# Kernel tuning notes

Hardware: AMD Instinct MI355X
Metric: run time of the kernel (lower is better)

## Reference

```python
import jax, jax.numpy as jnp
import numpy as np

ALPHA = 0.2
NEG = -9e15


def gat_layer(h, adj, W, a):
    # h: [B,N,Fin], adj: [B,N,N], W: [Fin,Fout], a: [2*Fout,1]
    Wh = jnp.matmul(h, W)                       # [B,N,Fout]
    Fout = W.shape[1]
    a1 = a[:Fout, 0]                             # source part
    a2 = a[Fout:, 0]                             # target part
    # e_ij = LeakyReLU(a1.Wh_i + a2.Wh_j) -- avoids O(N^2*2F) concat
    e = jax.nn.leaky_relu(
        (Wh @ a1)[:, :, None] + (Wh @ a2)[:, None, :], negative_slope=ALPHA
    )                                            # [B,N,N]
    att = jax.nn.softmax(jnp.where(adj > 0, e, NEG), axis=2)
    return jnp.matmul(att, Wh)                  # [B,N,Fout]


def setup_inputs() -> dict:
    key = jax.random.key(0)
    ks = jax.random.split(key, 6)
    B, N, F_IN, F_HID, F_OUT, H = 16, 1024, 256, 64, 64, 4
    x = jax.random.normal(ks[0], (B, N, F_IN), dtype=jnp.float32)
    adj = jax.random.randint(ks[1], (B, N, N), 0, 2, dtype=jnp.int32)
    W_heads = jax.random.normal(ks[2], (H, F_IN, F_HID), dtype=jnp.float32) * 0.1
    a_heads = jax.random.normal(ks[3], (H, 2 * F_HID, 1), dtype=jnp.float32) * 0.1
    W_out = jax.random.normal(ks[4], (H * F_HID, F_OUT), dtype=jnp.float32) * 0.1
    a_out = jax.random.normal(ks[5], (2 * F_OUT, 1), dtype=jnp.float32) * 0.1
    return {"x": x, "adj": adj, "W_heads": W_heads, "a_heads": a_heads,
            "W_out": W_out, "a_out": a_out}


def reference(x, adj, W_heads, a_heads, W_out, a_out):
    # multi-head: vmap over heads -> [H,B,N,F_hid]
    heads = jax.vmap(lambda W, a: gat_layer(x, adj, W, a))(W_heads, a_heads)
    H, B, N, Fh = heads.shape
    h_cat = jnp.transpose(heads, (1, 2, 0, 3)).reshape(B, N, H * Fh)
    out = jax.nn.elu(gat_layer(h_cat, adj, W_out, a_out))  # [B,N,nclass]
    return jnp.mean(out, axis=1)                           # [B,nclass]
```

## Files before the change

### kernel.cpp

```cpp
#include <hip/hip_runtime.h>
#include <math.h>

#define BB 16
#define NN 1024
#define FH 64
#define NH 4
#define LOG2E 1.4426950408889634f

typedef __attribute__((ext_vector_type(8))) short short8;
typedef __attribute__((ext_vector_type(4))) float f32x4;
typedef __attribute__((ext_vector_type(4))) unsigned u32x4;
typedef unsigned long long u64;
typedef unsigned short ushort_t;

__device__ inline unsigned f2bf(float x) {
    unsigned u = __builtin_bit_cast(unsigned, x);
    u += 0x7fff + ((u >> 16) & 1);
    return u >> 16;
}
__device__ inline unsigned pkbf(float lo, float hi) {
    unsigned r;
    asm("v_cvt_pk_bf16_f32 %0, %1, %2" : "=v"(r) : "v"(lo), "v"(hi));
    return r;
}
__device__ inline float bf2f(short v) {
    return __builtin_bit_cast(float, (unsigned)((unsigned short)v) << 16);
}

__global__ void pack_kernel(const int* __restrict__ adj, u64* __restrict__ bm,
                            const float* __restrict__ Whd, const float* __restrict__ Wo,
                            ushort_t* __restrict__ BT1, ushort_t* __restrict__ BT2,
                            float* __restrict__ outz) {
    const int row = blockIdx.x * 4 + (threadIdx.x >> 6);
    const int lane = threadIdx.x & 63;
    const int* __restrict__ ar = adj + (size_t)row * NN;
    #pragma unroll
    for (int g = 0; g < 16; ++g) {
        u64 m = __ballot(ar[g * 64 + lane] > 0);
        if (lane == 0) bm[row * 16 + g] = m;
    }
    const int col = blockIdx.x, k = threadIdx.x;
    if (col < 256)      BT1[col * 256 + k] = (ushort_t)f2bf(Whd[(col >> 6) * 16384 + k * 64 + (col & 63)]);
    else if (col < 320) BT2[(col - 256) * 256 + k] = (ushort_t)f2bf(Wo[k * 64 + (col - 256)]);
    if (col == 0) {
        #pragma unroll
        for (int i = 0; i < 4; ++i) outz[i * 256 + k] = 0.f;
    }
}

template <int A_BF16>
__global__ __launch_bounds__(256, 4) void gemm_fused(
    const void* __restrict__ Ap, const ushort_t* __restrict__ BT,
    const float* __restrict__ av, ushort_t* __restrict__ WhbT,
    float* __restrict__ s1, float* __restrict__ s2, const int S) {
    constexpr int K = 256;
    __shared__ __align__(16) short tbuf[64][72];
    const int tid = threadIdx.x;
    const int w = tid >> 6, l = tid & 63, lo = l & 15, kg = l >> 4;

    const int nx = gridDim.x;
    const int id = blockIdx.y * nx + blockIdx.x;
    const int nwg = nx * gridDim.y;
    const int lid = (id & 7) * (nwg >> 3) + (id >> 3);
    const int row0 = (lid / nx) * 64, col0 = (lid % nx) * 64;

    const int b = row0 >> 10, j0 = row0 & (NN - 1);
    const int hsel = col0 >> 6;

    f32x4 acc[4];
    #pragma unroll
    for (int cb = 0; cb < 4; ++cb) acc[cb] = (f32x4){0.f, 0.f, 0.f, 0.f};

    if (A_BF16) {
        const ushort_t* __restrict__ arow = (const ushort_t*)Ap + (size_t)(row0 + w * 16 + lo) * K;
        #pragma unroll
        for (int ks = 0; ks < 8; ++ks) {
            const int k0 = ks * 32 + kg * 8;
            const short8 af = *(const short8*)(arow + k0);
            #pragma unroll
            for (int cb = 0; cb < 4; ++cb) {
                const short8 bf = *(const short8*)(BT + (size_t)(col0 + cb * 16 + lo) * K + k0);
                acc[cb] = __builtin_amdgcn_mfma_f32_16x16x32_bf16(af, bf, acc[cb], 0, 0, 0);
            }
        }
    } else {
        const float* __restrict__ arow = (const float*)Ap + (size_t)(row0 + w * 16 + lo) * K;
        #pragma unroll
        for (int ks = 0; ks < 8; ++ks) {
            const int k0 = ks * 32 + kg * 8;
            const float4 a0 = *(const float4*)(arow + k0);
            const float4 a1 = *(const float4*)(arow + k0 + 4);
            u32x4 ap;
            ap[0] = pkbf(a0.x, a0.y); ap[1] = pkbf(a0.z, a0.w);
            ap[2] = pkbf(a1.x, a1.y); ap[3] = pkbf(a1.z, a1.w);
            const short8 af = __builtin_bit_cast(short8, ap);
            #pragma unroll
            for (int cb = 0; cb < 4; ++cb) {
                const short8 bf = *(const short8*)(BT + (size_t)(col0 + cb * 16 + lo) * K + k0);
                acc[cb] = __builtin_amdgcn_mfma_f32_16x16x32_bf16(af, bf, acc[cb], 0, 0, 0);
            }
        }
    }

    float a1v[4], a2v[4];
    #pragma unroll
    for (int cb = 0; cb < 4; ++cb) {
        a1v[cb] = av[hsel * 128 + cb * 16 + lo];
        a2v[cb] = av[hsel * 128 + 64 + cb * 16 + lo];
    }
    float sp1[4], sp2[4];
    #pragma unroll
    for (int r = 0; r < 4; ++r) {
        sp1[r] = acc[0][r] * a1v[0] + acc[1][r] * a1v[1] + acc[2][r] * a1v[2] + acc[3][r] * a1v[3];
        sp2[r] = acc[0][r] * a2v[0] + acc[1][r] * a2v[1] + acc[2][r] * a2v[2] + acc[3][r] * a2v[3];
    }
    #pragma unroll
    for (int m = 1; m < 16; m <<= 1) {
        #pragma unroll
        for (int r = 0; r < 4; ++r) {
            sp1[r] += __shfl_xor(sp1[r], m);
            sp2[r] += __shfl_xor(sp2[r], m);
        }
    }
    if (lo == 0) {
        #pragma unroll
        for (int r = 0; r < 4; ++r) {
            const int R = row0 + w * 16 + kg * 4 + r;
            s1[hsel * (BB * NN) + R] = sp1[r];
            s2[hsel * (BB * NN) + R] = sp2[r] * LOG2E;
        }
    }

    #pragma unroll
    for (int cb = 0; cb < 4; ++cb)
        #pragma unroll
        for (int rp = 0; rp < 2; ++rp)
            ((unsigned*)tbuf)[(cb * 16 + lo) * 36 + w * 8 + kg * 2 + rp] =
                pkbf(acc[cb][rp * 2], acc[cb][rp * 2 + 1]);
    __syncthreads();
    const int fl = tid >> 2, ch = tid & 3;
    const short8 v0 = *(const short8*)((const short*)tbuf + fl * 72 + ch * 16);
    const short8 v1 = *(const short8*)((const short*)tbuf + fl * 72 + ch * 16 + 8);
    ushort_t* dst = WhbT + ((size_t)(b * S) + col0 + fl) * NN + j0 + ch * 16;
    *(short8*)dst = v0;
    *(short8*)(dst + 8) = v1;
}

template <int H, int JQ, int OUT_BF16>
__global__ __launch_bounds__(256, 4) void apply_kernel(
    const ushort_t* __restrict__ WhbT, const int S,
    const float* __restrict__ s1, const float* __restrict__ s2,
    const unsigned* __restrict__ bm32,
    void* __restrict__ outp, float* __restrict__ sums) {
    constexpr int JLEN = NN / JQ;
    constexpr int BW = JLEN / 32;
    constexpr int NCH = JLEN / 64;
    constexpr int SB = 2 * 8192;
    constexpr int UBUF = SB;

    __shared__ __align__(16) float s2s[JLEN];
    __shared__ unsigned bs[64][BW + 1];
    __shared__ __align__(16) char ubuf[UBUF];
    auto stage = (unsigned (*)[64][32])ubuf;

    const int Bk = blockIdx.x;
    const int lid = (Bk & 7) * 128 + (Bk >> 3);
    const int it = lid & 15;
    const int b  = (lid >> 4) & 15;
    const int z  = lid >> 8;
    const int h  = (H > 1) ? z : 0;
    const int jq = (JQ > 1) ? z : 0;
    const int j0g = jq * JLEN;

    const int tid = threadIdx.x;
    const int w = tid >> 6, l = tid & 63;
    const int lo = l & 15, kg = l >> 4;
    const int iloc = w * 16 + lo;
    const int rbase = b * NN + it * 64;
    const int gi = rbase + iloc;
    const int hb = h * (BB * NN);

    const ushort_t* __restrict__ whb = WhbT + ((size_t)(b * S + h * FH)) * NN + j0g;

    const int r0 = tid >> 3, st = tid & 7;
    const int sw = (st ^ (r0 & 7)) * 4;
    const size_t ga = (size_t)r0 * NN + st * 8;
    const size_t gb = (size_t)(r0 + 32) * NN + st * 8;

    int4 cva0 = *(const int4*)(whb + ga);
    int4 cva1 = *(const int4*)(whb + gb);

    const float* __restrict__ s2g = s2 + hb + b * NN + j0g;
    for (int k = tid; k < JLEN / 4; k += 256)
        *(float4*)(s2s + k * 4) = *(const float4*)(s2g + k * 4);
    for (int idx = tid; idx < 64 * BW; idx += 256) {
        int r = idx / BW, wd = idx - r * BW;
        bs[r][wd] = bm32[(size_t)(rbase + r) * 32 + (j0g >> 5) + wd];
    }

    const float s1L = s1[hb + gi] * LOG2E;
    const float Arow = s1L;
    const float Brow = s1L * 0.2f;

    short8 ones;
    #pragma unroll
    for (int e = 0; e < 8; ++e) ones[e] = (short)0x3F80;

    f32x4 acc[4];
    #pragma unroll
    for (int fb = 0; fb < 4; ++fb) acc[fb] = (f32x4){0.f, 0.f, 0.f, 0.f};
    f32x4 accs = (f32x4){0.f, 0.f, 0.f, 0.f};

    *(int4*)&stage[0][r0][sw] = cva0;
    *(int4*)&stage[0][r0 + 32][sw] = cva1;
    if (1 < NCH) {
        cva0 = *(const int4*)(whb + 64 + ga);
        cva1 = *(const int4*)(whb + 64 + gb);
    }
    __syncthreads();

    #pragma unroll
    for (int c = 0; c < NCH; ++c) {
        int4 cvb0, cvb1;
        if (c + 2 < NCH) {
            const ushort_t* src = whb + (c + 2) * 64;
            cvb0 = *(const int4*)(src + ga);
            cvb1 = *(const int4*)(src + gb);
        }
        #pragma unroll
        for (int ks = 0; ks < 2; ++ks) {
            const int kb = c * 64 + ks * 32 + kg * 8;
            const unsigned byte = (bs[iloc][c * 2 + ks] >> (kg * 8)) & 0xFF;
            const float4 sa = *(const float4*)(s2s + kb);
            const float4 sb = *(const float4*)(s2s + kb + 4);
            const float s2r[8] = {sa.x, sa.y, sa.z, sa.w, sb.x, sb.y, sb.z, sb.w};
            float pv[8];
            #pragma unroll
            for (int e = 0; e < 8; ++e) {
                const float t = s2r[e];
                const float u = Arow + t;
                const float v = __builtin_fmaf(t, 0.2f, Brow);
                float ev = fmaxf(u, v);
                ev = ((byte >> e) & 1) ? ev : -1.0e5f;
                pv[e] = __builtin_amdgcn_exp2f(ev);
            }
            u32x4 pk;
            pk[0] = pkbf(pv[0], pv[1]); pk[1] = pkbf(pv[2], pv[3]);
            pk[2] = pkbf(pv[4], pv[5]); pk[3] = pkbf(pv[6], pv[7]);
            const short8 bfr = __builtin_bit_cast(short8, pk);
            __builtin_amdgcn_s_setprio(1);
            #pragma unroll
            for (int fb = 0; fb < 4; ++fb) {
                const int row = fb * 16 + lo;
                const int slot = (ks * 4 + kg) ^ (row & 7);
                const short8 afr = *(const short8*)&stage[c & 1][row][slot * 4];
                acc[fb] = __builtin_amdgcn_mfma_f32_16x16x32_bf16(afr, bfr, acc[fb], 0, 0, 0);
            }
            accs = __builtin_amdgcn_mfma_f32_16x16x32_bf16(ones, bfr, accs, 0, 0, 0);
            __builtin_amdgcn_s_setprio(0);
        }
        if (c + 1 < NCH) {
            *(int4*)&stage[(c + 1) & 1][r0][sw] = cva0;
            *(int4*)&stage[(c + 1) & 1][r0 + 32][sw] = cva1;
        }
        cva0 = cvb0;
        cva1 = cvb1;
        __syncthreads();
    }

    const float inv = OUT_BF16 ? (1.0f / accs[0]) : 1.0f;
    if (!OUT_BF16 && kg == 0)
        sums[(size_t)jq * (BB * NN) + rbase + iloc] = accs[0];

    unsigned* ot = (unsigned*)ubuf;
    #pragma unroll
    for (int fb = 0; fb < 4; ++fb)
        #pragma unroll
        for (int rp = 0; rp < 2; ++rp)
            ot[iloc * 36 + fb * 8 + kg * 2 + rp] =
                pkbf(acc[fb][rp * 2] * inv, acc[fb][rp * 2 + 1] * inv);
    __syncthreads();
    const int i2 = tid >> 2, ch = tid & 3;
    const short8 v0 = *(const short8*)((const short*)ubuf + i2 * 72 + ch * 16);
    const short8 v1 = *(const short8*)((const short*)ubuf + i2 * 72 + ch * 16 + 8);
    if constexpr (OUT_BF16) {
        ushort_t* dst = (ushort_t*)outp + (size_t)(b * NN + it * 64 + i2) * 256 + h * FH + ch * 16;
        *(short8*)dst = v0;
        *(short8*)(dst + 8) = v1;
    } else {
        ushort_t* dst = (ushort_t*)outp + (size_t)jq * (BB * NN * FH)
                      + (size_t)(b * NN + it * 64 + i2) * FH + ch * 16;
        *(short8*)dst = v0;
        *(short8*)(dst + 8) = v1;
    }
}

__global__ __launch_bounds__(256) void mean1_kernel(const ushort_t* __restrict__ part,
                                                    const float* __restrict__ sums,
                                                    float* __restrict__ out) {
    const int b = blockIdx.x, ck = blockIdx.y;
    const int tid = threadIdx.x;
    const int f = tid & 63, g = tid >> 6;
    float acc = 0.f;
    #pragma unroll
    for (int i = g; i < 64; i += 4) {
        const int row = b * NN + ck * 64 + i;
        const float srow = sums[row] + sums[row + 16384]
                         + sums[row + 32768] + sums[row + 49152];
        float v = 0.f;
        #pragma unroll
        for (int q = 0; q < 4; ++q)
            v += bf2f((short)part[(size_t)q * 1048576 + (size_t)row * FH + f]);
        v /= srow;
        v = (v > 0.f) ? v : (__builtin_amdgcn_exp2f(v * LOG2E) - 1.0f);
        acc += v;
    }
    __shared__ float r[4][64];
    r[g][f] = acc;
    __syncthreads();
    if (g == 0)
        atomicAdd(&out[b * FH + f],
                  (r[0][f] + r[1][f] + r[2][f] + r[3][f]) * (1.0f / NN));
}

extern "C" void kernel_launch(void* const* d_in, const int* in_sizes, int n_in,
                              void* d_out, int out_size, void* d_ws, size_t ws_size,
                              hipStream_t stream) {
    const float* x       = (const float*)d_in[0];
    const int*   adj     = (const int*)d_in[1];
    const float* W_heads = (const float*)d_in[2];
    const float* a_heads = (const float*)d_in[3];
    const float* W_out   = (const float*)d_in[4];
    const float* a_out   = (const float*)d_in[5];
    float* out = (float*)d_out;
    float* f0  = (float*)d_ws;

    ushort_t* hcat  = (ushort_t*)f0;
    ushort_t* part  = (ushort_t*)f0;
    ushort_t* WhbT1 = (ushort_t*)(f0 + 2097152);
    ushort_t* WhbT2 = (ushort_t*)(f0 + 4194304);
    u64*      bmask = (u64*)(f0 + 4718592);
    ushort_t* WbT1  = (ushort_t*)(f0 + 5242880);
    ushort_t* WbT2  = (ushort_t*)(f0 + 5275648);
    float*    s1_1  = f0 + 5283840;
    float*    s2_1  = s1_1 + 65536;
    float*    s1_2  = s2_1 + 65536;
    float*    s2_2  = s1_2 + 16384;
    float*    sums2 = s2_2 + 16384;

    dim3 blk(256);

    pack_kernel<<<dim3(BB * NN / 4), blk, 0, stream>>>(adj, bmask, W_heads, W_out,
                                                       WbT1, WbT2, out);

    gemm_fused<0><<<dim3(4, 256), blk, 0, stream>>>(x, WbT1, a_heads, WhbT1, s1_1, s2_1, 256);
    apply_kernel<NH, 1, 1><<<dim3(1024), blk, 0, stream>>>(WhbT1, 256, s1_1, s2_1,
                                                           (const unsigned*)bmask, hcat, nullptr);

    gemm_fused<1><<<dim3(1, 256), blk, 0, stream>>>(hcat, WbT2, a_out, WhbT2, s1_2, s2_2, 64);
    apply_kernel<1, 4, 0><<<dim3(1024), blk, 0, stream>>>(WhbT2, 64, s1_2, s2_2,
                                                          (const unsigned*)bmask, part, sums2);

    mean1_kernel<<<dim3(BB, 16), blk, 0, stream>>>(part, sums2, out);
}
```

Before: 94.25 us.

## Fuse adjacency bitmask packing into first-layer GEMM kernel

The adjacency-to-bitmask packing moves out of the standalone pack kernel and into the first gemm_fused launch. Each of its 1024 workgroups packs 16 rows, so all 16384 rows are covered. Odd workgroups pack before their GEMM and even ones after it, so the adjacency reads (64 MB of int32) can overlap with MFMA work. The now-small weight pack runs in its own 320-block kernel. This removes a separate bandwidth-bound pass, at the cost of more register pressure and longer-running GEMM workgroups.

```diff
diff --git a/kernel.cpp b/kernel.cpp
--- a/kernel.cpp
+++ b/kernel.cpp
@@ -27,18 +27,9 @@
     return __builtin_bit_cast(float, (unsigned)((unsigned short)v) << 16);
 }
 
-__global__ void pack_kernel(const int* __restrict__ adj, u64* __restrict__ bm,
-                            const float* __restrict__ Whd, const float* __restrict__ Wo,
-                            ushort_t* __restrict__ BT1, ushort_t* __restrict__ BT2,
-                            float* __restrict__ outz) {
-    const int row = blockIdx.x * 4 + (threadIdx.x >> 6);
-    const int lane = threadIdx.x & 63;
-    const int* __restrict__ ar = adj + (size_t)row * NN;
-    #pragma unroll
-    for (int g = 0; g < 16; ++g) {
-        u64 m = __ballot(ar[g * 64 + lane] > 0);
-        if (lane == 0) bm[row * 16 + g] = m;
-    }
+__global__ void packw_kernel(const float* __restrict__ Whd, const float* __restrict__ Wo,
+                             ushort_t* __restrict__ BT1, ushort_t* __restrict__ BT2,
+                             float* __restrict__ outz) {
     const int col = blockIdx.x, k = threadIdx.x;
     if (col < 256)      BT1[col * 256 + k] = (ushort_t)f2bf(Whd[(col >> 6) * 16384 + k * 64 + (col & 63)]);
     else if (col < 320) BT2[(col - 256) * 256 + k] = (ushort_t)f2bf(Wo[k * 64 + (col - 256)]);
@@ -48,11 +39,12 @@
     }
 }
 
-template <int A_BF16>
+template <int A_BF16, int PACK>
 __global__ __launch_bounds__(256, 4) void gemm_fused(
     const void* __restrict__ Ap, const ushort_t* __restrict__ BT,
     const float* __restrict__ av, ushort_t* __restrict__ WhbT,
-    float* __restrict__ s1, float* __restrict__ s2, const int S) {
+    float* __restrict__ s1, float* __restrict__ s2, const int S,
+    const int* __restrict__ adj, u64* __restrict__ bm) {
     constexpr int K = 256;
     __shared__ __align__(16) short tbuf[64][72];
     const int tid = threadIdx.x;
@@ -66,6 +58,23 @@
 
     const int b = row0 >> 10, j0 = row0 & (NN - 1);
     const int hsel = col0 >> 6;
+
+    auto do_pack = [&]() {
+        const int rowb = id * 16 + w * 4;
+        const int* __restrict__ ar = adj + (size_t)rowb * NN;
+        #pragma unroll
+        for (int rr = 0; rr < 4; ++rr) {
+            int va[16];
+            #pragma unroll
+            for (int g = 0; g < 16; ++g) va[g] = ar[(size_t)rr * NN + g * 64 + l];
+            #pragma unroll
+            for (int g = 0; g < 16; ++g) {
+                u64 m = __ballot(va[g] > 0);
+                if (l == 0) bm[(rowb + rr) * 16 + g] = m;
+            }
+        }
+    };
+    if constexpr (PACK) { if (id & 1) do_pack(); }
 
     f32x4 acc[4];
     #pragma unroll
@@ -144,6 +153,8 @@
     ushort_t* dst = WhbT + ((size_t)(b * S) + col0 + fl) * NN + j0 + ch * 16;
     *(short8*)dst = v0;
     *(short8*)(dst + 8) = v1;
+
+    if constexpr (PACK) { if (!(id & 1)) do_pack(); }
 }
 
 template <int H, int JQ, int OUT_BF16>
@@ -350,14 +361,15 @@
 
     dim3 blk(256);
 
-    pack_kernel<<<dim3(BB * NN / 4), blk, 0, stream>>>(adj, bmask, W_heads, W_out,
-                                                       WbT1, WbT2, out);
-
-    gemm_fused<0><<<dim3(4, 256), blk, 0, stream>>>(x, WbT1, a_heads, WhbT1, s1_1, s2_1, 256);
+    packw_kernel<<<dim3(320), blk, 0, stream>>>(W_heads, W_out, WbT1, WbT2, out);
+
+    gemm_fused<0, 1><<<dim3(4, 256), blk, 0, stream>>>(x, WbT1, a_heads, WhbT1, s1_1, s2_1, 256,
+                                                       adj, bmask);
     apply_kernel<NH, 1, 1><<<dim3(1024), blk, 0, stream>>>(WhbT1, 256, s1_1, s2_1,
                                                            (const unsigned*)bmask, hcat, nullptr);
 
-    gemm_fused<1><<<dim3(1, 256), blk, 0, stream>>>(hcat, WbT2, a_out, WhbT2, s1_2, s2_2, 64);
+    gemm_fused<1, 0><<<dim3(1, 256), blk, 0, stream>>>(hcat, WbT2, a_out, WhbT2, s1_2, s2_2, 64,
+                                                       nullptr, nullptr);
     apply_kernel<1, 4, 0><<<dim3(1024), blk, 0, stream>>>(WhbT2, 64, s1_2, s2_2,
                                                           (const unsigned*)bmask, part, sums2);
 
```

Measured after the change: 93.86 us. About the same (-0.4%).
